# Kernel tuning notes

Hardware: AMD Instinct MI355X
Metric: run time of the kernel (lower is better)

Reference implementation:

```python
import jax, jax.numpy as jnp
import numpy as np

EMBED_DIM = 1024
NUM_HEADS = 16
HEAD_DIM = EMBED_DIM // NUM_HEADS


def setup_inputs() -> dict:
    key = jax.random.key(0)
    ks = jax.random.split(key, 9)
    s = 1.0 / np.sqrt(EMBED_DIM)
    x = jax.random.normal(ks[0], (4, 2048, EMBED_DIM), dtype=jnp.float32)
    # torch.nn.Linear weights are [out_features, in_features]
    Wq = jax.random.uniform(ks[1], (EMBED_DIM, EMBED_DIM), jnp.float32, -s, s)
    bq = jax.random.uniform(ks[2], (EMBED_DIM,), jnp.float32, -s, s)
    Wk = jax.random.uniform(ks[3], (EMBED_DIM, EMBED_DIM), jnp.float32, -s, s)
    bk = jax.random.uniform(ks[4], (EMBED_DIM,), jnp.float32, -s, s)
    Wv = jax.random.uniform(ks[5], (EMBED_DIM, EMBED_DIM), jnp.float32, -s, s)
    bv = jax.random.uniform(ks[6], (EMBED_DIM,), jnp.float32, -s, s)
    Wo = jax.random.uniform(ks[7], (EMBED_DIM, EMBED_DIM), jnp.float32, -s, s)
    bo = jax.random.uniform(ks[8], (EMBED_DIM,), jnp.float32, -s, s)
    return {"x": x, "Wq": Wq, "bq": bq, "Wk": Wk, "bk": bk,
            "Wv": Wv, "bv": bv, "Wo": Wo, "bo": bo}


def reference(x, Wq, bq, Wk, bk, Wv, bv, Wo, bo):
    B, S, E = x.shape
    H, D = NUM_HEADS, HEAD_DIM

    def proj(W, b):
        y = jnp.einsum('bse,fe->bsf', x, W) + b          # Linear: x @ W.T + b
        return y.reshape(B, S, H, D).transpose(0, 2, 1, 3)  # [B,H,S,D]

    q = proj(Wq, bq)
    k = proj(Wk, bk)
    v = proj(Wv, bv)

    scores = jnp.einsum('bhqd,bhkd->bhqk', q, k) / jnp.sqrt(jnp.float32(D))
    attn = jax.nn.soft_sign(scores)                      # softsign, no normalization
    # dropout p=0.0 -> identity
    ctx = jnp.einsum('bhqk,bhkd->bhqd', attn, v)         # [B,H,S,D]
    ctx = ctx.transpose(0, 2, 1, 3).reshape(B, S, E)
    out = jnp.einsum('bse,fe->bsf', ctx, Wo) + bo
    return (out,)
```

## Files before the change

kernel.cpp:

```cpp
#include <hip/hip_runtime.h>
#include <hip/hip_bf16.h>
#include <stdint.h>

#define Bb 4
#define SEQ 2048
#define Ee 1024
#define Hh 16
#define Dh 64
#define Mm (Bb*SEQ)

typedef __attribute__((ext_vector_type(8))) short bfrag;
typedef __attribute__((ext_vector_type(4))) float f32x4;
typedef __attribute__((ext_vector_type(16))) float f32x16;
typedef __attribute__((ext_vector_type(4))) unsigned u32x4;
typedef unsigned short u16;

__device__ __forceinline__ u16 f2bf(float x) {
  __hip_bfloat16 h = __float2bfloat16(x);
  return *reinterpret_cast<u16*>(&h);
}

__device__ __forceinline__ void gll16(const void* g, void* l) {
  __builtin_amdgcn_global_load_lds(
      (const __attribute__((address_space(1))) void*)g,
      (__attribute__((address_space(3))) void*)l, 16, 0, 0);
}

__global__ __launch_bounds__(256) void cast_all(
    const float* __restrict__ x,  const float* __restrict__ wq,
    const float* __restrict__ wk, const float* __restrict__ wv,
    const float* __restrict__ wo,
    u16* __restrict__ xb, u16* __restrict__ wqb, u16* __restrict__ wkb,
    u16* __restrict__ wvb, u16* __restrict__ wob)
{
  int idx = blockIdx.x * 256 + threadIdx.x;
  const float* src; u16* dst; int off;
  if (idx < 2097152) { src = x; dst = xb; off = idx; }
  else {
    int t = idx - 2097152;
    int seg = t >> 18;
    off = t & 262143;
    src = (seg == 0) ? wq : (seg == 1) ? wk : (seg == 2) ? wv : wo;
    dst = (seg == 0) ? wqb : (seg == 1) ? wkb : (seg == 2) ? wvb : wob;
  }
  float4 v = reinterpret_cast<const float4*>(src)[off];
  ushort4 o;
  o.x = f2bf(v.x); o.y = f2bf(v.y); o.z = f2bf(v.z); o.w = f2bf(v.w);
  reinterpret_cast<ushort4*>(dst)[off] = o;
}

template<int OUTMODE>
__global__ __launch_bounds__(256) void gemm_bt(
    const u16* __restrict__ A,
    const u16* __restrict__ W0, const u16* __restrict__ W1, const u16* __restrict__ W2,
    const float* __restrict__ b0, const float* __restrict__ b1, const float* __restrict__ b2,
    void* __restrict__ outp, int K, int N)
{
  __shared__ __align__(16) u16 smem[16384];
  u16* As = smem;
  u16* Bs = smem + 8192;
  const int tid  = threadIdx.x;
  const int lane = tid & 63;
  const int wid  = tid >> 6;
  const int bm = blockIdx.x * 128;
  const int bn = blockIdx.y * 128;
  const int z  = blockIdx.z;
  const u16*  Wp = (z == 0) ? W0 : (z == 1) ? W1 : W2;
  const float* bp = (z == 0) ? b0 : (z == 1) ? b1 : b2;
  const int wr = (wid >> 1) * 64, wc = (wid & 1) * 64;
  const int lr = lane & 15, lk = (lane >> 4) * 8;
  f32x4 acc[4][4] = {};

  for (int kt = 0; kt < K; kt += 64) {
    __syncthreads();
#pragma unroll
    for (int p = 0; p < 4; ++p) {
      int flat = p * 2048 + tid * 8;
      int r = flat >> 6, c = flat & 63;
      gll16(A + (size_t)(bm + r) * K + kt + c, As + flat);
    }
#pragma unroll
    for (int p = 0; p < 4; ++p) {
      int flat = p * 2048 + tid * 8;
      int r = flat >> 6, c = flat & 63;
      gll16(Wp + (size_t)(bn + r) * K + kt + c, Bs + flat);
    }
    __syncthreads();
#pragma unroll
    for (int kk = 0; kk < 2; ++kk) {
      bfrag a[4], b[4];
#pragma unroll
      for (int i = 0; i < 4; ++i)
        a[i] = *reinterpret_cast<const bfrag*>(&As[(wr + i * 16 + lr) * 64 + kk * 32 + lk]);
#pragma unroll
      for (int j = 0; j < 4; ++j)
        b[j] = *reinterpret_cast<const bfrag*>(&Bs[(wc + j * 16 + lr) * 64 + kk * 32 + lk]);
#pragma unroll
      for (int i = 0; i < 4; ++i)
#pragma unroll
        for (int j = 0; j < 4; ++j)
          acc[i][j] = __builtin_amdgcn_mfma_f32_16x16x32_bf16(a[i], b[j], acc[i][j], 0, 0, 0);
    }
  }

  float bias[4];
#pragma unroll
  for (int j = 0; j < 4; ++j) bias[j] = bp[bn + wc + j * 16 + (lane & 15)];

  if (OUTMODE == 0) {
    const float scl = (z == 0) ? 0.125f : 1.0f;
    __syncthreads();
    u16* cst = smem;
#pragma unroll
    for (int i = 0; i < 4; ++i)
#pragma unroll
      for (int j = 0; j < 4; ++j)
#pragma unroll
        for (int e = 0; e < 4; ++e)
          cst[(wr + i * 16 + (lane >> 4) * 4 + e) * 128 + wc + j * 16 + (lane & 15)] =
              f2bf((acc[i][j][e] + bias[j]) * scl);
    __syncthreads();
    u16* outb = (u16*)outp + (size_t)z * (size_t)Mm * Ee;
#pragma unroll
    for (int p = 0; p < 8; ++p) {
      int chunk = p * 256 + tid;
      int r = chunk >> 4;
      int c = (chunk & 15) * 8;
      int m = bm + r, f = bn + c;
      u16* dst = outb + ((((size_t)(m >> 11) * Hh + (f >> 6)) * SEQ + (m & 2047)) * Dh + (f & 63));
      *reinterpret_cast<bfrag*>(dst) = *reinterpret_cast<const bfrag*>(&cst[r * 128 + c]);
    }
  } else {
    float* outf = (float*)outp;
    float* cf = reinterpret_cast<float*>(smem);
#pragma unroll
    for (int half = 0; half < 2; ++half) {
      __syncthreads();
      if ((wid >> 1) == half) {
#pragma unroll
        for (int i = 0; i < 4; ++i)
#pragma unroll
          for (int j = 0; j < 4; ++j)
#pragma unroll
            for (int e = 0; e < 4; ++e)
              cf[(i * 16 + (lane >> 4) * 4 + e) * 128 + wc + j * 16 + (lane & 15)] =
                  acc[i][j][e] + bias[j];
      }
      __syncthreads();
#pragma unroll
      for (int p = 0; p < 8; ++p) {
        int chunk = p * 256 + tid;
        int r = chunk >> 5;
        int c = (chunk & 31) * 4;
        *reinterpret_cast<float4*>(&outf[(size_t)(bm + half * 64 + r) * N + bn + c]) =
            *reinterpret_cast<const float4*>(&cf[r * 128 + c]);
      }
    }
  }
}

__global__ __launch_bounds__(256) void transpose_v(const u16* __restrict__ v,
                                                   u16* __restrict__ vt)
{
  __shared__ __align__(16) u16 lds[8192];
  const int tid = threadIdx.x;
  const int bh = blockIdx.y;
  const int st = blockIdx.x * 128;
  const u16* vb = v + (size_t)bh * SEQ * Dh;
#pragma unroll
  for (int p = 0; p < 4; ++p) {
    int flat = p * 2048 + tid * 8;
    int s = flat >> 6, dp = flat & 63;
    int dl = dp ^ (((s >> 3) & 7) << 3);
    gll16(vb + (size_t)(st + s) * Dh + dl, lds + flat);
  }
  __syncthreads();
  u16* vtb = vt + (size_t)bh * Dh * SEQ;
#pragma unroll
  for (int p = 0; p < 4; ++p) {
    int chunk = p * 256 + tid;
    int sc = chunk & 15, d = chunk >> 4;
    bfrag o;
#pragma unroll
    for (int e = 0; e < 8; ++e) {
      int sp = sc * 8 + e;
      int ss = (sp & ~12) | ((sp & 4) << 1) | ((sp & 8) >> 1);
      int X = ((ss >> 3) & 7) << 3;
      o[e] = (short)lds[ss * 64 + (d ^ X)];
    }
    *reinterpret_cast<bfrag*>(&vtb[(size_t)d * SEQ + st + sc * 8]) = o;
  }
}

__global__ __launch_bounds__(256, 4) void attn_kernel(
    const u16* __restrict__ qg_, const u16* __restrict__ kg,
    const u16* __restrict__ vtg, u16* __restrict__ ctx)
{
  __shared__ __align__(16) u16 smem[16384];
  const int tid  = threadIdx.x;
  const int lane = tid & 63;
  const int wid  = tid >> 6;
  const int ql = lane & 31;
  const int hi = lane >> 5;

  const int orig = blockIdx.x;
  const int swz  = (orig & 7) * 128 + (orig >> 3);
  const int bh = swz >> 4;
  const int q0 = (swz & 15) * 128;

  const u16* qb  = qg_ + (size_t)bh * SEQ * Dh;
  const u16* kb  = kg  + (size_t)bh * SEQ * Dh;
  const u16* vtb = vtg + (size_t)bh * Dh * SEQ;

  bfrag qf[4];
#pragma unroll
  for (int db = 0; db < 4; ++db)
    qf[db] = *reinterpret_cast<const bfrag*>(
        &qb[(size_t)(q0 + wid * 32 + ql) * Dh + db * 16 + hi * 8]);

  int koff[2], voff[2];
#pragma unroll
  for (int p = 0; p < 2; ++p) {
    int f = p * 2048 + tid * 8;
    int lrow = f >> 7;
    int log7 = (f & 127) ^ ((lrow & 15) << 3);
    int r = lrow * 2 + (log7 >> 6);
    int c = log7 & 63;
    koff[p] = r * 64 + c;
    voff[p] = r * SEQ + c;
  }

  f32x16 o[2] = {};

  auto stage = [&](int kt, int buf) {
#pragma unroll
    for (int p = 0; p < 2; ++p)
      gll16(kb + (size_t)kt * 64 + koff[p], smem + buf * 4096 + p * 2048 + tid * 8);
#pragma unroll
    for (int p = 0; p < 2; ++p)
      gll16(vtb + kt + voff[p], smem + 8192 + buf * 4096 + p * 2048 + tid * 8);
  };

  stage(0, 0);
  __syncthreads();

  for (int ti = 0; ti < 32; ++ti) {
    const int cur = ti & 1;
    if (ti < 31) stage((ti + 1) * 64, cur ^ 1);
    const u16* Kb = smem + cur * 4096;
    const u16* Vb = smem + 8192 + cur * 4096;

#pragma unroll
    for (int kh = 0; kh < 2; ++kh) {
      f32x16 s = {};
      __builtin_amdgcn_s_setprio(1);
#pragma unroll
      for (int db = 0; db < 4; ++db) {
        const int krow = kh * 32 + ql;
        const int lr2 = krow >> 1;
        const int log7 = ((krow & 1) << 6) | (db * 16 + hi * 8);
        bfrag ka = *reinterpret_cast<const bfrag*>(
            &Kb[lr2 * 128 + (log7 ^ ((lr2 & 15) << 3))]);
        s = __builtin_amdgcn_mfma_f32_32x32x16_bf16(ka, qf[db], s, 0, 0, 0);
      }
      __builtin_amdgcn_s_setprio(0);

      unsigned pw[8];
#pragma unroll
      for (int r = 0; r < 8; ++r) {
        float a = s[2 * r], b = s[2 * r + 1];
        float pa_ = a * __builtin_amdgcn_rcpf(1.0f + __builtin_fabsf(a));
        float pb_ = b * __builtin_amdgcn_rcpf(1.0f + __builtin_fabsf(b));
        pw[r] = __builtin_amdgcn_perm(__builtin_bit_cast(unsigned, pb_),
                                      __builtin_bit_cast(unsigned, pa_),
                                      0x07060302u);
      }
      u32x4 w0 = {pw[0], pw[1], pw[2], pw[3]};
      u32x4 w1 = {pw[4], pw[5], pw[6], pw[7]};
      bfrag pa0 = __builtin_bit_cast(bfrag, w0);
      bfrag pa1 = __builtin_bit_cast(bfrag, w1);

      __builtin_amdgcn_s_setprio(1);
#pragma unroll
      for (int tt = 0; tt < 2; ++tt)
#pragma unroll
        for (int dh = 0; dh < 2; ++dh) {
          const int vrow = dh * 32 + ql;
          const int lr2 = vrow >> 1;
          const int log7 = ((vrow & 1) << 6) | (kh * 32 + tt * 16 + hi * 8);
          bfrag vb = *reinterpret_cast<const bfrag*>(
              &Vb[lr2 * 128 + (log7 ^ ((lr2 & 15) << 3))]);
          o[dh] = __builtin_amdgcn_mfma_f32_32x32x16_bf16(tt ? pa1 : pa0, vb, o[dh], 0, 0, 0);
        }
      __builtin_amdgcn_s_setprio(0);
    }
    __syncthreads();
  }

  u16* cst = smem;
#pragma unroll
  for (int dh = 0; dh < 2; ++dh)
#pragma unroll
    for (int r = 0; r < 16; ++r) {
      int qrow = wid * 32 + (r & 3) + 8 * (r >> 2) + 4 * hi;
      cst[qrow * 64 + dh * 32 + ql] = f2bf(o[dh][r]);
    }
  __syncthreads();
  const int b = bh >> 4, h = bh & 15;
#pragma unroll
  for (int p = 0; p < 4; ++p) {
    int chunk = p * 256 + tid;
    int r = chunk >> 3, cc = (chunk & 7) * 8;
    u16* dst = ctx + ((size_t)(b * SEQ + q0 + r) * Ee + h * Dh + cc);
    *reinterpret_cast<bfrag*>(dst) = *reinterpret_cast<const bfrag*>(&cst[r * 64 + cc]);
  }
}

extern "C" void kernel_launch(void* const* d_in, const int* in_sizes, int n_in,
                              void* d_out, int out_size, void* d_ws, size_t ws_size,
                              hipStream_t stream)
{
  const float* x  = (const float*)d_in[0];
  const float* Wq = (const float*)d_in[1];
  const float* bq = (const float*)d_in[2];
  const float* Wk = (const float*)d_in[3];
  const float* bk = (const float*)d_in[4];
  const float* Wv = (const float*)d_in[5];
  const float* bv = (const float*)d_in[6];
  const float* Wo = (const float*)d_in[7];
  const float* bo = (const float*)d_in[8];
  float* out = (float*)d_out;

  u16* ws  = (u16*)d_ws;
  u16* xb  = ws;
  u16* wqb = ws + 8388608;
  u16* wkb = wqb + 1048576;
  u16* wvb = wkb + 1048576;
  u16* wob = wvb + 1048576;
  u16* qkv = wob + 1048576;
  u16* q_  = qkv;
  u16* k_  = qkv + 8388608;
  u16* v_  = qkv + 2 * 8388608;
  u16* vt  = xb;
  u16* ctx = v_;

  cast_all<<<12288, 256, 0, stream>>>(x, Wq, Wk, Wv, Wo, xb, wqb, wkb, wvb, wob);

  gemm_bt<0><<<dim3(64, 8, 3), 256, 0, stream>>>(xb, wqb, wkb, wvb, bq, bk, bv,
                                                 qkv, Ee, Ee);
  transpose_v<<<dim3(16, 64), 256, 0, stream>>>(v_, vt);
  attn_kernel<<<1024, 256, 0, stream>>>(q_, k_, vt, ctx);
  gemm_bt<1><<<dim3(64, 8, 1), 256, 0, stream>>>(ctx, wob, wob, wob, bo, bo, bo,
                                                 out, Ee, Ee);
}
```

Baseline: 299.4 us.

## Double-buffer GEMM LDS, swizzle tiles, and fuse V transpose into QKV epilogue

The GEMM main loop now double-buffers its LDS tiles, so the next k-tile loads while MFMAs run on the current one, with one barrier per iteration. The LDS layout gets an XOR swizzle to cut bank conflicts, and s_setprio is raised around the MFMA block. The separate transpose_v kernel is removed: the V projection writes V transposed straight from its LDS epilogue, which saves a kernel launch and a round trip through global memory. Doubling LDS to 64KB per block may lower occupancy, and the transposed epilogue reads LDS in a gather pattern.

```diff
diff --git a/kernel.cpp b/kernel.cpp
--- a/kernel.cpp
+++ b/kernel.cpp
@@ -54,11 +54,9 @@
     const u16* __restrict__ A,
     const u16* __restrict__ W0, const u16* __restrict__ W1, const u16* __restrict__ W2,
     const float* __restrict__ b0, const float* __restrict__ b1, const float* __restrict__ b2,
-    void* __restrict__ outp, int K, int N)
+    void* __restrict__ outp, u16* __restrict__ vt, int K, int N)
 {
-  __shared__ __align__(16) u16 smem[16384];
-  u16* As = smem;
-  u16* Bs = smem + 8192;
+  __shared__ __align__(16) u16 smem[32768];
   const int tid  = threadIdx.x;
   const int lane = tid & 63;
   const int wid  = tid >> 6;
@@ -69,38 +67,58 @@
   const float* bp = (z == 0) ? b0 : (z == 1) ? b1 : b2;
   const int wr = (wid >> 1) * 64, wc = (wid & 1) * 64;
   const int lr = lane & 15, lk = (lane >> 4) * 8;
+  const int kx = (lr & 7) << 3;
+
+  size_t aoff[4], boff[4];
+#pragma unroll
+  for (int p = 0; p < 4; ++p) {
+    int flat = p * 2048 + tid * 8;
+    int r = flat >> 6, c = flat & 63;
+    int cs = c ^ ((r & 7) << 3);
+    aoff[p] = (size_t)(bm + r) * K + cs;
+    boff[p] = (size_t)(bn + r) * K + cs;
+  }
+
   f32x4 acc[4][4] = {};
 
-  for (int kt = 0; kt < K; kt += 64) {
-    __syncthreads();
-#pragma unroll
-    for (int p = 0; p < 4; ++p) {
-      int flat = p * 2048 + tid * 8;
-      int r = flat >> 6, c = flat & 63;
-      gll16(A + (size_t)(bm + r) * K + kt + c, As + flat);
-    }
-#pragma unroll
-    for (int p = 0; p < 4; ++p) {
-      int flat = p * 2048 + tid * 8;
-      int r = flat >> 6, c = flat & 63;
-      gll16(Wp + (size_t)(bn + r) * K + kt + c, Bs + flat);
-    }
-    __syncthreads();
+  auto stage = [&](int kt, int s) {
+    u16* As = smem + s * 16384;
+    u16* Bs = As + 8192;
+#pragma unroll
+    for (int p = 0; p < 4; ++p)
+      gll16(A + aoff[p] + kt, As + p * 2048 + tid * 8);
+#pragma unroll
+    for (int p = 0; p < 4; ++p)
+      gll16(Wp + boff[p] + kt, Bs + p * 2048 + tid * 8);
+  };
+
+  const int NT = K >> 6;
+  stage(0, 0);
+  __syncthreads();
+  for (int t = 0; t < NT; ++t) {
+    const int cur = t & 1;
+    if (t + 1 < NT) stage((t + 1) << 6, cur ^ 1);
+    const u16* As = smem + cur * 16384;
+    const u16* Bs = As + 8192;
 #pragma unroll
     for (int kk = 0; kk < 2; ++kk) {
       bfrag a[4], b[4];
+      const int col = (kk * 32 + lk) ^ kx;
 #pragma unroll
       for (int i = 0; i < 4; ++i)
-        a[i] = *reinterpret_cast<const bfrag*>(&As[(wr + i * 16 + lr) * 64 + kk * 32 + lk]);
+        a[i] = *reinterpret_cast<const bfrag*>(&As[(wr + i * 16 + lr) * 64 + col]);
 #pragma unroll
       for (int j = 0; j < 4; ++j)
-        b[j] = *reinterpret_cast<const bfrag*>(&Bs[(wc + j * 16 + lr) * 64 + kk * 32 + lk]);
+        b[j] = *reinterpret_cast<const bfrag*>(&Bs[(wc + j * 16 + lr) * 64 + col]);
+      __builtin_amdgcn_s_setprio(1);
 #pragma unroll
       for (int i = 0; i < 4; ++i)
 #pragma unroll
         for (int j = 0; j < 4; ++j)
           acc[i][j] = __builtin_amdgcn_mfma_f32_16x16x32_bf16(a[i], b[j], acc[i][j], 0, 0, 0);
-    }
+      __builtin_amdgcn_s_setprio(0);
+    }
+    __syncthreads();
   }
 
   float bias[4];
@@ -109,26 +127,49 @@
 
   if (OUTMODE == 0) {
     const float scl = (z == 0) ? 0.125f : 1.0f;
+    u16* cst = smem;
+#pragma unroll
+    for (int i = 0; i < 4; ++i)
+#pragma unroll
+      for (int j = 0; j < 4; ++j)
+#pragma unroll
+        for (int e = 0; e < 4; ++e) {
+          int row = wr + i * 16 + (lane >> 4) * 4 + e;
+          int c2  = wc + j * 16 + (lane & 15);
+          cst[row * 128 + (c2 ^ ((row & 7) << 3))] = f2bf((acc[i][j][e] + bias[j]) * scl);
+        }
     __syncthreads();
-    u16* cst = smem;
-#pragma unroll
-    for (int i = 0; i < 4; ++i)
-#pragma unroll
-      for (int j = 0; j < 4; ++j)
-#pragma unroll
-        for (int e = 0; e < 4; ++e)
-          cst[(wr + i * 16 + (lane >> 4) * 4 + e) * 128 + wc + j * 16 + (lane & 15)] =
-              f2bf((acc[i][j][e] + bias[j]) * scl);
-    __syncthreads();
-    u16* outb = (u16*)outp + (size_t)z * (size_t)Mm * Ee;
-#pragma unroll
-    for (int p = 0; p < 8; ++p) {
-      int chunk = p * 256 + tid;
-      int r = chunk >> 4;
-      int c = (chunk & 15) * 8;
-      int m = bm + r, f = bn + c;
-      u16* dst = outb + ((((size_t)(m >> 11) * Hh + (f >> 6)) * SEQ + (m & 2047)) * Dh + (f & 63));
-      *reinterpret_cast<bfrag*>(dst) = *reinterpret_cast<const bfrag*>(&cst[r * 128 + c]);
+    if (z < 2) {
+      u16* outb = (u16*)outp + (size_t)z * (size_t)Mm * Ee;
+#pragma unroll
+      for (int p = 0; p < 8; ++p) {
+        int chunk = p * 256 + tid;
+        int r = chunk >> 4;
+        int c = (chunk & 15) * 8;
+        int m = bm + r, f = bn + c;
+        u16* dst = outb + ((((size_t)(m >> 11) * Hh + (f >> 6)) * SEQ + (m & 2047)) * Dh + (f & 63));
+        *reinterpret_cast<bfrag*>(dst) =
+            *reinterpret_cast<const bfrag*>(&cst[r * 128 + (c ^ ((r & 7) << 3))]);
+      }
+    } else {
+      const int bq = bm >> 11;
+      const int s_base = bm & 2047;
+#pragma unroll
+      for (int p = 0; p < 8; ++p) {
+        int chunk = p * 256 + tid;
+        int d = chunk >> 4, sc = chunk & 15;
+        int f = bn + d;
+        int h = f >> 6, dl = f & 63;
+        bfrag o;
+#pragma unroll
+        for (int e = 0; e < 8; ++e) {
+          int sp = sc * 8 + e;
+          int ss = (sp & ~12) | ((sp & 4) << 1) | ((sp & 8) >> 1);
+          o[e] = (short)cst[ss * 128 + (d ^ ((ss & 7) << 3))];
+        }
+        *reinterpret_cast<bfrag*>(
+            &vt[((size_t)((bq * Hh + h) * Dh + dl)) * SEQ + s_base + sc * 8]) = o;
+      }
     }
   } else {
     float* outf = (float*)outp;
@@ -156,39 +197,6 @@
             *reinterpret_cast<const float4*>(&cf[r * 128 + c]);
       }
     }
-  }
-}
-
-__global__ __launch_bounds__(256) void transpose_v(const u16* __restrict__ v,
-                                                   u16* __restrict__ vt)
-{
-  __shared__ __align__(16) u16 lds[8192];
-  const int tid = threadIdx.x;
-  const int bh = blockIdx.y;
-  const int st = blockIdx.x * 128;
-  const u16* vb = v + (size_t)bh * SEQ * Dh;
-#pragma unroll
-  for (int p = 0; p < 4; ++p) {
-    int flat = p * 2048 + tid * 8;
-    int s = flat >> 6, dp = flat & 63;
-    int dl = dp ^ (((s >> 3) & 7) << 3);
-    gll16(vb + (size_t)(st + s) * Dh + dl, lds + flat);
-  }
-  __syncthreads();
-  u16* vtb = vt + (size_t)bh * Dh * SEQ;
-#pragma unroll
-  for (int p = 0; p < 4; ++p) {
-    int chunk = p * 256 + tid;
-    int sc = chunk & 15, d = chunk >> 4;
-    bfrag o;
-#pragma unroll
-    for (int e = 0; e < 8; ++e) {
-      int sp = sc * 8 + e;
-      int ss = (sp & ~12) | ((sp & 4) << 1) | ((sp & 8) >> 1);
-      int X = ((ss >> 3) & 7) << 3;
-      o[e] = (short)lds[ss * 64 + (d ^ X)];
-    }
-    *reinterpret_cast<bfrag*>(&vtb[(size_t)d * SEQ + st + sc * 8]) = o;
   }
 }
 
@@ -340,16 +348,14 @@
   u16* qkv = wob + 1048576;
   u16* q_  = qkv;
   u16* k_  = qkv + 8388608;
-  u16* v_  = qkv + 2 * 8388608;
-  u16* vt  = xb;
-  u16* ctx = v_;
+  u16* vt  = qkv + 2 * 8388608;
+  u16* ctx = xb;
 
   cast_all<<<12288, 256, 0, stream>>>(x, Wq, Wk, Wv, Wo, xb, wqb, wkb, wvb, wob);
 
   gemm_bt<0><<<dim3(64, 8, 3), 256, 0, stream>>>(xb, wqb, wkb, wvb, bq, bk, bv,
-                                                 qkv, Ee, Ee);
-  transpose_v<<<dim3(16, 64), 256, 0, stream>>>(v_, vt);
+                                                 qkv, vt, Ee, Ee);
   attn_kernel<<<1024, 256, 0, stream>>>(q_, k_, vt, ctx);
   gemm_bt<1><<<dim3(64, 8, 1), 256, 0, stream>>>(ctx, wob, wob, wob, bo, bo, bo,
-                                                 out, Ee, Ee);
-}
+                                                 out, nullptr, Ee, Ee);
+}
```

New measurement: 256.0 us. 1.17x faster.
